# Performance work log

Measured on AMD Instinct MI355X. Metric: run time of the kernel, lower is better.

The kernel has to match this reference:

```python
import jax, jax.numpy as jnp
import numpy as np

WIN_SIZE = 11
WIN_SIGMA = 1.5
DATA_RANGE = 1.0
K1, K2 = 0.01, 0.03


def _gauss_1d(size, sigma):
    coords = np.arange(size, dtype=np.float64) - size // 2
    g = np.exp(-(coords ** 2) / (2.0 * sigma ** 2))
    g = g / g.sum()
    return jnp.asarray(g, dtype=jnp.float32)


def _gaussian_filter(x, win1d):
    # x: (N, C, H, W); separable depthwise gaussian blur, VALID padding
    C = x.shape[1]
    dn = ('NCHW', 'OIHW', 'NCHW')
    kh = jnp.tile(win1d.reshape(1, 1, -1, 1), (C, 1, 1, 1))
    kw = jnp.tile(win1d.reshape(1, 1, 1, -1), (C, 1, 1, 1))
    x = jax.lax.conv_general_dilated(x, kh, (1, 1), 'VALID', dimension_numbers=dn, feature_group_count=C)
    x = jax.lax.conv_general_dilated(x, kw, (1, 1), 'VALID', dimension_numbers=dn, feature_group_count=C)
    return x


def setup_inputs() -> dict:
    key = jax.random.key(0)
    k1, k2 = jax.random.split(key)
    shape = (32, 1, 512, 512)
    y_pred = jax.random.uniform(k1, shape, dtype=jnp.float32)
    y_true = jax.random.uniform(k2, shape, dtype=jnp.float32)
    return {"y_pred": y_pred, "y_true": y_true}


def reference(y_pred, y_true):
    # SSIMLoss.forward: 1 - ssim(y_true, y_pred, data_range=1.0, size_average=True)
    C1 = (K1 * DATA_RANGE) ** 2
    C2 = (K2 * DATA_RANGE) ** 2
    win = _gauss_1d(WIN_SIZE, WIN_SIGMA)

    X, Y = y_true, y_pred
    mu1 = _gaussian_filter(X, win)
    mu2 = _gaussian_filter(Y, win)
    sigma1_sq = _gaussian_filter(X * X, win) - mu1 * mu1
    sigma2_sq = _gaussian_filter(Y * Y, win) - mu2 * mu2
    sigma12 = _gaussian_filter(X * Y, win) - mu1 * mu2

    cs_map = (2.0 * sigma12 + C2) / (sigma1_sq + sigma2_sq + C2)
    ssim_map = ((2.0 * mu1 * mu2 + C1) / (mu1 * mu1 + mu2 * mu2 + C1)) * cs_map
    # size_average=True -> mean over everything
    return 1.0 - jnp.mean(ssim_map)
```

## Files before the change

### kernel.cpp

```cpp
#include <hip/hip_runtime.h>
#include <cmath>

#define IMG      512
#define OUT      502
#define TW       64
#define TH       32
#define IW       74
#define P2       78
#define NTHREADS 256
#define TILES_X  8
#define TILES_Y  16
#define NIMG     32
#define NBLOCKS  (TILES_X * TILES_Y * NIMG)

struct GaussW { float w[11]; };

__global__ __launch_bounds__(NTHREADS, 4)
void ssim_tile_kernel(const float* __restrict__ ypred,
                      const float* __restrict__ ytrue,
                      float* __restrict__ partials,
                      GaussW gw)
{
    __shared__ __align__(16) float2 sXY[TH * P2];
    __shared__ __align__(16) float2 sSP[TH * P2];
    __shared__ float wsum[4];

    const int t     = threadIdx.x;
    const int tileX = blockIdx.x, tileY = blockIdx.y, img = blockIdx.z;
    const int ox0 = (tileX == TILES_X - 1) ? (OUT - TW) : tileX * TW;
    const int oy0 = (tileY == TILES_Y - 1) ? (OUT - TH) : tileY * TH;

    const size_t imgoff = (size_t)img * (IMG * IMG);
    const float* __restrict__ Xp = ytrue + imgoff;
    const float* __restrict__ Yp = ypred + imgoff;

    if (t < IW * 3) {
        const int c  = t % IW;
        const int g  = t / IW;
        const int r0 = g * 11;

        const unsigned off0 = (unsigned)((oy0 + r0) * IMG + (ox0 + c));

        float xv[21], yv[21];
        #pragma unroll
        for (int k = 0; k < 20; ++k) {
            xv[k] = Xp[off0 + k * IMG];
            yv[k] = Yp[off0 + k * IMG];
        }
        {
            const unsigned o20 = (g < 2) ? (off0 + 20 * IMG) : off0;
            xv[20] = Xp[o20];
            yv[20] = Yp[o20];
        }

        float aX[11], aY[11], aS[11], aP[11];
        #pragma unroll
        for (int j = 0; j < 11; ++j) { aX[j] = 0.f; aY[j] = 0.f; aS[j] = 0.f; aP[j] = 0.f; }

        #pragma unroll
        for (int k = 0; k < 20; ++k) {
            const float x = xv[k];
            const float y = yv[k];
            const float s = __builtin_fmaf(y, y, x * x);
            const float p = x * y;
            #pragma unroll
            for (int j = 0; j < 11; ++j) {
                if (k - j >= 0 && k - j <= 10) {
                    const float w = gw.w[k - j];
                    aX[j] += w * x;
                    aY[j] += w * y;
                    aS[j] += w * s;
                    aP[j] += w * p;
                }
            }
        }
        if (g < 2) {
            const float x = xv[20];
            const float y = yv[20];
            const float w = gw.w[10];
            aX[10] += w * x;
            aY[10] += w * y;
            aS[10] += w * __builtin_fmaf(y, y, x * x);
            aP[10] += w * (x * y);
        }

        const int o0 = r0 * P2 + c;
        #pragma unroll
        for (int j = 0; j < 10; ++j) {
            const int o = o0 + j * P2;
            sXY[o] = make_float2(aX[j], aY[j]);
            sSP[o] = make_float2(aS[j], aP[j]);
        }
        if (g < 2) {
            const int o = o0 + 10 * P2;
            sXY[o] = make_float2(aX[10], aY[10]);
            sSP[o] = make_float2(aS[10], aP[10]);
        }
    }
    __syncthreads();

    const float C1 = 0.0001f;
    const float C2 = 0.0009f;

    const int row  = t & 31;
    const int seg  = t >> 5;
    const int base = row * P2 + seg * 8;

    float winA[18], winB[18];

    {
        const float4* q = reinterpret_cast<const float4*>(&sXY[base]);
        #pragma unroll
        for (int i = 0; i < 9; ++i) {
            const float4 v = q[i];
            winA[2*i]     = v.x;  winB[2*i]     = v.y;
            winA[2*i + 1] = v.z;  winB[2*i + 1] = v.w;
        }
    }
    float mu1v[8], mu2v[8];
    #pragma unroll
    for (int c = 0; c < 8; ++c) {
        float r1 = 0.f, r2 = 0.f;
        #pragma unroll
        for (int k = 0; k < 11; ++k) {
            const float w = gw.w[k];
            r1 += w * winA[c + k];
            r2 += w * winB[c + k];
        }
        mu1v[c] = r1; mu2v[c] = r2;
    }

    {
        const float4* q = reinterpret_cast<const float4*>(&sSP[base]);
        #pragma unroll
        for (int i = 0; i < 9; ++i) {
            const float4 v = q[i];
            winA[2*i]     = v.x;  winB[2*i]     = v.y;
            winA[2*i + 1] = v.z;  winB[2*i + 1] = v.w;
        }
    }

    const int  oy     = oy0 + row;
    const bool rowown = (oy >= tileY * TH);
    float lsum = 0.f;

    #pragma unroll
    for (int c = 0; c < 8; ++c) {
        float b3 = 0.f, b4 = 0.f;
        #pragma unroll
        for (int k = 0; k < 11; ++k) {
            const float w = gw.w[k];
            b3 += w * winA[c + k];
            b4 += w * winB[c + k];
        }
        const int  ox  = ox0 + seg * 8 + c;
        const bool own = rowown && (ox >= tileX * TW);
        const float mu1 = mu1v[c], mu2 = mu2v[c];
        const float Pm  = mu1 * mu2;
        const float Sm  = __builtin_fmaf(mu1, mu1, mu2 * mu2);
        const float num = __builtin_fmaf(2.f, Pm, C1) * __builtin_fmaf(2.f, b4 - Pm, C2);
        const float den = (Sm + C1) * ((b3 + C2) - Sm);
        const float ssim = num * __builtin_amdgcn_rcpf(den);
        lsum += own ? ssim : 0.f;
    }

    #pragma unroll
    for (int off = 32; off > 0; off >>= 1) lsum += __shfl_down(lsum, off, 64);
    if ((t & 63) == 0) wsum[t >> 6] = lsum;
    __syncthreads();
    if (t == 0) {
        const float b = wsum[0] + wsum[1] + wsum[2] + wsum[3];
        partials[((size_t)img * TILES_Y + tileY) * TILES_X + tileX] = b;
    }
}

__global__ void ssim_reduce_kernel(const float* __restrict__ partials,
                                   float* __restrict__ out)
{
    __shared__ double ws[4];
    const int t = threadIdx.x;
    double s = 0.0;
    for (int i = t; i < NBLOCKS; i += 256) s += (double)partials[i];
    #pragma unroll
    for (int off = 32; off > 0; off >>= 1) s += __shfl_down(s, off, 64);
    if ((t & 63) == 0) ws[t >> 6] = s;
    __syncthreads();
    if (t == 0) {
        const double total = ws[0] + ws[1] + ws[2] + ws[3];
        const double mean  = total / ((double)OUT * (double)OUT * (double)NIMG);
        out[0] = (float)(1.0 - mean);
    }
}

extern "C" void kernel_launch(void* const* d_in, const int* in_sizes, int n_in,
                              void* d_out, int out_size, void* d_ws, size_t ws_size,
                              hipStream_t stream)
{
    const float* ypred = (const float*)d_in[0];
    const float* ytrue = (const float*)d_in[1];
    float* out      = (float*)d_out;
    float* partials = (float*)d_ws;

    GaussW gw;
    double g[11], sum = 0.0;
    for (int i = 0; i < 11; ++i) {
        const double c = (double)i - 5.0;
        g[i] = std::exp(-(c * c) / (2.0 * 1.5 * 1.5));
        sum += g[i];
    }
    for (int i = 0; i < 11; ++i) gw.w[i] = (float)(g[i] / sum);

    dim3 grid(TILES_X, TILES_Y, NIMG);
    ssim_tile_kernel<<<grid, NTHREADS, 0, stream>>>(ypred, ytrue, partials, gw);
    ssim_reduce_kernel<<<1, 256, 0, stream>>>(partials, out);
}
```

Before: 116.1 us.

## Split tile pass into two phases sharing one LDS buffer to raise occupancy

The vertical blur pass is split into two phases: first X/Y blurred into a single shared buffer and consumed for mu, then the squared/product channels recomputed from re-read global inputs into the same buffer. This halves LDS use and cuts register pressure (no 21-element input arrays, only two accumulator sets at a time), and launch bounds rise from 4 to 6 blocks per SIMD for higher occupancy. In exchange, each tile reads its inputs from global memory twice, likely hitting in cache, and adds an extra barrier.

```diff
diff --git a/kernel.cpp b/kernel.cpp
--- a/kernel.cpp
+++ b/kernel.cpp
@@ -15,14 +15,13 @@
 
 struct GaussW { float w[11]; };
 
-__global__ __launch_bounds__(NTHREADS, 4)
+__global__ __launch_bounds__(NTHREADS, 6)
 void ssim_tile_kernel(const float* __restrict__ ypred,
                       const float* __restrict__ ytrue,
                       float* __restrict__ partials,
                       GaussW gw)
 {
-    __shared__ __align__(16) float2 sXY[TH * P2];
-    __shared__ __align__(16) float2 sSP[TH * P2];
+    __shared__ __align__(16) float2 sP[TH * P2];
     __shared__ float wsum[4];
 
     const int t     = threadIdx.x;
@@ -34,109 +33,116 @@
     const float* __restrict__ Xp = ytrue + imgoff;
     const float* __restrict__ Yp = ypred + imgoff;
 
-    if (t < IW * 3) {
-        const int c  = t % IW;
-        const int g  = t / IW;
-        const int r0 = g * 11;
-
-        const unsigned off0 = (unsigned)((oy0 + r0) * IMG + (ox0 + c));
-
-        float xv[21], yv[21];
+    const bool p1   = (t < IW * 3);
+    const int  c    = t % IW;
+    const int  g    = t / IW;
+    const int  r0   = g * 11;
+    const unsigned off0 = (unsigned)((oy0 + r0) * IMG + (ox0 + c));
+    const int  o0   = r0 * P2 + c;
+
+    const int row    = t & 31;
+    const int seg    = t >> 5;
+    const int basef2 = row * P2 + seg * 8;
+
+    if (p1) {
+        float aX[11], aY[11];
+        #pragma unroll
+        for (int j = 0; j < 11; ++j) { aX[j] = 0.f; aY[j] = 0.f; }
+
         #pragma unroll
         for (int k = 0; k < 20; ++k) {
-            xv[k] = Xp[off0 + k * IMG];
-            yv[k] = Yp[off0 + k * IMG];
-        }
-        {
-            const unsigned o20 = (g < 2) ? (off0 + 20 * IMG) : off0;
-            xv[20] = Xp[o20];
-            yv[20] = Yp[o20];
-        }
-
-        float aX[11], aY[11], aS[11], aP[11];
-        #pragma unroll
-        for (int j = 0; j < 11; ++j) { aX[j] = 0.f; aY[j] = 0.f; aS[j] = 0.f; aP[j] = 0.f; }
+            const float x = Xp[off0 + k * IMG];
+            const float y = Yp[off0 + k * IMG];
+            #pragma unroll
+            for (int j = 0; j < 11; ++j) {
+                if (k - j >= 0 && k - j <= 10) {
+                    const float w = gw.w[k - j];
+                    aX[j] = __builtin_fmaf(w, x, aX[j]);
+                    aY[j] = __builtin_fmaf(w, y, aY[j]);
+                }
+            }
+        }
+        if (g < 2) {
+            const float x = Xp[off0 + 20 * IMG];
+            const float y = Yp[off0 + 20 * IMG];
+            aX[10] = __builtin_fmaf(gw.w[10], x, aX[10]);
+            aY[10] = __builtin_fmaf(gw.w[10], y, aY[10]);
+        }
+
+        #pragma unroll
+        for (int j = 0; j < 10; ++j) sP[o0 + j * P2] = make_float2(aX[j], aY[j]);
+        if (g < 2)                   sP[o0 + 10 * P2] = make_float2(aX[10], aY[10]);
+    }
+    __syncthreads();
+
+    float mu1[8], mu2[8];
+    {
+        float wA[18], wB[18];
+        const float4* q = reinterpret_cast<const float4*>(&sP[basef2]);
+        #pragma unroll
+        for (int i = 0; i < 9; ++i) {
+            const float4 v = q[i];
+            wA[2*i] = v.x;  wB[2*i] = v.y;
+            wA[2*i+1] = v.z;  wB[2*i+1] = v.w;
+        }
+        #pragma unroll
+        for (int cc = 0; cc < 8; ++cc) {
+            float r1 = 0.f, r2 = 0.f;
+            #pragma unroll
+            for (int k = 0; k < 11; ++k) {
+                const float w = gw.w[k];
+                r1 = __builtin_fmaf(w, wA[cc + k], r1);
+                r2 = __builtin_fmaf(w, wB[cc + k], r2);
+            }
+            mu1[cc] = r1; mu2[cc] = r2;
+        }
+    }
+    __syncthreads();
+
+    if (p1) {
+        float aS[11], aP[11];
+        #pragma unroll
+        for (int j = 0; j < 11; ++j) { aS[j] = 0.f; aP[j] = 0.f; }
 
         #pragma unroll
         for (int k = 0; k < 20; ++k) {
-            const float x = xv[k];
-            const float y = yv[k];
+            const float x = Xp[off0 + k * IMG];
+            const float y = Yp[off0 + k * IMG];
             const float s = __builtin_fmaf(y, y, x * x);
             const float p = x * y;
             #pragma unroll
             for (int j = 0; j < 11; ++j) {
                 if (k - j >= 0 && k - j <= 10) {
                     const float w = gw.w[k - j];
-                    aX[j] += w * x;
-                    aY[j] += w * y;
-                    aS[j] += w * s;
-                    aP[j] += w * p;
+                    aS[j] = __builtin_fmaf(w, s, aS[j]);
+                    aP[j] = __builtin_fmaf(w, p, aP[j]);
                 }
             }
         }
         if (g < 2) {
-            const float x = xv[20];
-            const float y = yv[20];
-            const float w = gw.w[10];
-            aX[10] += w * x;
-            aY[10] += w * y;
-            aS[10] += w * __builtin_fmaf(y, y, x * x);
-            aP[10] += w * (x * y);
-        }
-
-        const int o0 = r0 * P2 + c;
-        #pragma unroll
-        for (int j = 0; j < 10; ++j) {
-            const int o = o0 + j * P2;
-            sXY[o] = make_float2(aX[j], aY[j]);
-            sSP[o] = make_float2(aS[j], aP[j]);
-        }
-        if (g < 2) {
-            const int o = o0 + 10 * P2;
-            sXY[o] = make_float2(aX[10], aY[10]);
-            sSP[o] = make_float2(aS[10], aP[10]);
-        }
+            const float x = Xp[off0 + 20 * IMG];
+            const float y = Yp[off0 + 20 * IMG];
+            aS[10] = __builtin_fmaf(gw.w[10], __builtin_fmaf(y, y, x * x), aS[10]);
+            aP[10] = __builtin_fmaf(gw.w[10], x * y, aP[10]);
+        }
+
+        #pragma unroll
+        for (int j = 0; j < 10; ++j) sP[o0 + j * P2] = make_float2(aS[j], aP[j]);
+        if (g < 2)                   sP[o0 + 10 * P2] = make_float2(aS[10], aP[10]);
     }
     __syncthreads();
 
     const float C1 = 0.0001f;
     const float C2 = 0.0009f;
 
-    const int row  = t & 31;
-    const int seg  = t >> 5;
-    const int base = row * P2 + seg * 8;
-
-    float winA[18], winB[18];
-
+    float wA[18], wB[18];
     {
-        const float4* q = reinterpret_cast<const float4*>(&sXY[base]);
+        const float4* q = reinterpret_cast<const float4*>(&sP[basef2]);
         #pragma unroll
         for (int i = 0; i < 9; ++i) {
             const float4 v = q[i];
-            winA[2*i]     = v.x;  winB[2*i]     = v.y;
-            winA[2*i + 1] = v.z;  winB[2*i + 1] = v.w;
-        }
-    }
-    float mu1v[8], mu2v[8];
-    #pragma unroll
-    for (int c = 0; c < 8; ++c) {
-        float r1 = 0.f, r2 = 0.f;
-        #pragma unroll
-        for (int k = 0; k < 11; ++k) {
-            const float w = gw.w[k];
-            r1 += w * winA[c + k];
-            r2 += w * winB[c + k];
-        }
-        mu1v[c] = r1; mu2v[c] = r2;
-    }
-
-    {
-        const float4* q = reinterpret_cast<const float4*>(&sSP[base]);
-        #pragma unroll
-        for (int i = 0; i < 9; ++i) {
-            const float4 v = q[i];
-            winA[2*i]     = v.x;  winB[2*i]     = v.y;
-            winA[2*i + 1] = v.z;  winB[2*i + 1] = v.w;
+            wA[2*i] = v.x;  wB[2*i] = v.y;
+            wA[2*i+1] = v.z;  wB[2*i+1] = v.w;
         }
     }
 
@@ -145,19 +151,19 @@
     float lsum = 0.f;
 
     #pragma unroll
-    for (int c = 0; c < 8; ++c) {
+    for (int cc = 0; cc < 8; ++cc) {
         float b3 = 0.f, b4 = 0.f;
         #pragma unroll
         for (int k = 0; k < 11; ++k) {
             const float w = gw.w[k];
-            b3 += w * winA[c + k];
-            b4 += w * winB[c + k];
-        }
-        const int  ox  = ox0 + seg * 8 + c;
+            b3 = __builtin_fmaf(w, wA[cc + k], b3);
+            b4 = __builtin_fmaf(w, wB[cc + k], b4);
+        }
+        const int  ox  = ox0 + seg * 8 + cc;
         const bool own = rowown && (ox >= tileX * TW);
-        const float mu1 = mu1v[c], mu2 = mu2v[c];
-        const float Pm  = mu1 * mu2;
-        const float Sm  = __builtin_fmaf(mu1, mu1, mu2 * mu2);
+        const float m1 = mu1[cc], m2 = mu2[cc];
+        const float Pm = m1 * m2;
+        const float Sm = __builtin_fmaf(m1, m1, m2 * m2);
         const float num = __builtin_fmaf(2.f, Pm, C1) * __builtin_fmaf(2.f, b4 - Pm, C2);
         const float den = (Sm + C1) * ((b3 + C2) - Sm);
         const float ssim = num * __builtin_amdgcn_rcpf(den);
```

New measurement: 134.0 us. 1.15x slower.
